# Performance work log

Measured on AMD Instinct MI355X. Metric: run time of the kernel, lower is better.

Reference implementation:

```python
import jax, jax.numpy as jnp
import numpy as np

B = 8192
N_CLASSES = 1024
MARGIN = 0.1
THRESH = 0.5
SCALE_POS = 2.0
SCALE_NEG = 40.0
EPS = 1e-5


def setup_inputs() -> dict:
    key = jax.random.key(0)
    k1, k2 = jax.random.split(key)
    # cosine-similarity-like values in [-1, 1]
    sim_mat = jax.random.uniform(k1, (B, B), dtype=jnp.float32, minval=-1.0, maxval=1.0)
    labels = jax.random.randint(k2, (B,), 0, N_CLASSES, dtype=jnp.int64)
    return {"sim_mat": sim_mat, "labels": labels}


def reference(sim_mat, labels):
    # [B, B] pair masks
    same = labels[:, None] == labels[None, :]
    pos_mask = same & (sim_mat < 1.0 - EPS)        # positives, excluding self-sim ~ 1
    neg_mask = ~same

    # per-row hardest positive (min) / hardest negative (max); inf sentinels when empty
    min_pos = jnp.min(jnp.where(pos_mask, sim_mat, jnp.inf), axis=1)   # [B]
    max_neg = jnp.max(jnp.where(neg_mask, sim_mat, -jnp.inf), axis=1)  # [B]

    # pair mining: keep informative pairs only
    sel_neg = neg_mask & (sim_mat + MARGIN > min_pos[:, None])
    sel_pos = pos_mask & (sim_mat - MARGIN < max_neg[:, None])

    valid = jnp.any(sel_neg, axis=1) & jnp.any(sel_pos, axis=1)  # rows contributing to loss

    # masked soft-plus style logsumexp losses (sim bounded in [-1,1], exp is safe)
    pos_sum = jnp.sum(jnp.where(sel_pos, jnp.exp(-SCALE_POS * (sim_mat - THRESH)), 0.0), axis=1)
    neg_sum = jnp.sum(jnp.where(sel_neg, jnp.exp(SCALE_NEG * (sim_mat - THRESH)), 0.0), axis=1)
    pos_loss = jnp.log1p(pos_sum) / SCALE_POS
    neg_loss = jnp.log1p(neg_sum) / SCALE_NEG

    loss = jnp.sum(jnp.where(valid, pos_loss + neg_loss, 0.0)) / sim_mat.shape[0]
    return loss
```

## Files before the change

kernel.cpp:

```cpp
#include <hip/hip_runtime.h>
#include <math.h>

namespace {
constexpr int   kB       = 8192;
constexpr int   kBlock   = 256;
constexpr int   kWaves   = kBlock / 64;
constexpr int   kRPW     = 2;
constexpr int   kGrid    = kB / (kWaves * kRPW);
constexpr int   kChunks  = kB / (64 * 4);
constexpr int   kNWaves  = kGrid * kWaves;
constexpr float kMargin   = 0.1f;
constexpr float kThresh   = 0.5f;
constexpr float kScalePos = 2.0f;
constexpr float kScaleNeg = 40.0f;
constexpr float kEps      = 1e-5f;
}

__global__ __launch_bounds__(kBlock, 2) void ms_rows_kernel(
    const float* __restrict__ sim,
    const int*   __restrict__ labels,
    float*       __restrict__ ws)
{
  const int tid  = threadIdx.x;
  const int wave = tid >> 6;
  const int lane = tid & 63;
  const int wid  = blockIdx.x * kWaves + wave;

  float wave_loss = 0.0f;

  #pragma unroll
  for (int rr = 0; rr < kRPW; ++rr) {
    const int row = wid * kRPW + rr;
    const int ml  = labels[row];
    const float* __restrict__ srow = sim + (size_t)row * kB;

    float4 buf[kChunks];
    #pragma unroll
    for (int k = 0; k < kChunks; ++k)
      buf[k] = *reinterpret_cast<const float4*>(srow + k * 256 + lane * 4);

    unsigned int msk[kChunks / 8] = {0, 0, 0, 0};
    float min_pos =  INFINITY;
    float max_neg = -INFINITY;
    #pragma unroll
    for (int k = 0; k < kChunks; ++k) {
      const int4   l4 = *reinterpret_cast<const int4*>(labels + k * 256 + lane * 4);
      const float4 v  = buf[k];
      const float xs[4] = {v.x, v.y, v.z, v.w};
      const int   ls[4] = {l4.x, l4.y, l4.z, l4.w};
      #pragma unroll
      for (int c = 0; c < 4; ++c) {
        const bool  same = (ls[c] == ml);
        msk[k >> 3] |= (unsigned)same << ((k & 7) * 4 + c);
        const float x = xs[c];
        min_pos = fminf(min_pos, (same && x < 1.0f - kEps) ? x : INFINITY);
        max_neg = fmaxf(max_neg, same ? -INFINITY : x);
      }
    }
    #pragma unroll
    for (int off = 32; off > 0; off >>= 1) {
      min_pos = fminf(min_pos, __shfl_xor(min_pos, off, 64));
      max_neg = fmaxf(max_neg, __shfl_xor(max_neg, off, 64));
    }

    float ps = 0.0f, ns = 0.0f;
    #pragma unroll
    for (int k = 0; k < kChunks; ++k) {
      const float4 v = buf[k];
      const float xs[4] = {v.x, v.y, v.z, v.w};
      #pragma unroll
      for (int c = 0; c < 4; ++c) {
        const bool  same = (msk[k >> 3] >> ((k & 7) * 4 + c)) & 1u;
        const float x = xs[c];
        const float a = same ? -kScalePos : kScaleNeg;
        const float e = __expf(a * (x - kThresh));
        ps += (same && x < 1.0f - kEps && x - kMargin < max_neg) ? e : 0.0f;
        ns += (!same && x + kMargin > min_pos) ? e : 0.0f;
      }
    }
    #pragma unroll
    for (int off = 32; off > 0; off >>= 1) {
      ps += __shfl_xor(ps, off, 64);
      ns += __shfl_xor(ns, off, 64);
    }
    if (ps > 0.0f && ns > 0.0f) {
      wave_loss += log1pf(ps) * (1.0f / kScalePos)
                 + log1pf(ns) * (1.0f / kScaleNeg);
    }
  }

  if (lane == 0) ws[wid] = wave_loss;
}

__global__ __launch_bounds__(256) void ms_reduce_kernel(
    const float* __restrict__ ws, float* __restrict__ out)
{
  const int tid = threadIdx.x;
  float s = 0.0f;
  #pragma unroll
  for (int i = tid; i < kNWaves; i += 256) s += ws[i];
  #pragma unroll
  for (int off = 32; off > 0; off >>= 1) s += __shfl_xor(s, off, 64);
  __shared__ float sm[4];
  if ((tid & 63) == 0) sm[tid >> 6] = s;
  __syncthreads();
  if (tid == 0)
    out[0] = (sm[0] + sm[1] + sm[2] + sm[3]) * (1.0f / (float)kB);
}

extern "C" void kernel_launch(void* const* d_in, const int* in_sizes, int n_in,
                              void* d_out, int out_size, void* d_ws, size_t ws_size,
                              hipStream_t stream) {
  const float* sim    = (const float*)d_in[0];
  const int*   labels = (const int*)d_in[1];
  float*       ws     = (float*)d_ws;
  float*       out    = (float*)d_out;

  ms_rows_kernel<<<dim3(kGrid), dim3(kBlock), 0, stream>>>(sim, labels, ws);
  ms_reduce_kernel<<<dim3(1), dim3(256), 0, stream>>>(ws, out);
}
```

Measured before the change: 432.9 us.

## Stream rows in double-buffered chunks and re-read them instead of holding whole rows

Each wave previously held an entire 8192-element row in registers (32 float4 per lane) across two passes. Now it handles one row, streams it in double-buffered chunks of 8 float4 for the min/max pass, then reloads the row from memory (likely L2/MALL hits) for the exp-sum pass. This cuts VGPR pressure so occupancy can rise (launch bounds raised to 4 blocks). The cost is reading the 256MB matrix twice, which doubles traffic if the reread misses cache.

```diff
diff --git a/kernel.cpp b/kernel.cpp
--- a/kernel.cpp
+++ b/kernel.cpp
@@ -5,10 +5,10 @@
 constexpr int   kB       = 8192;
 constexpr int   kBlock   = 256;
 constexpr int   kWaves   = kBlock / 64;
-constexpr int   kRPW     = 2;
-constexpr int   kGrid    = kB / (kWaves * kRPW);
-constexpr int   kChunks  = kB / (64 * 4);
-constexpr int   kNWaves  = kGrid * kWaves;
+constexpr int   kGrid    = kB / kWaves;
+constexpr int   kCF4     = 8;
+constexpr int   kChunkE  = 64 * 4 * kCF4;
+constexpr int   kNChunk  = kB / kChunkE;
 constexpr float kMargin   = 0.1f;
 constexpr float kThresh   = 0.5f;
 constexpr float kScalePos = 2.0f;
@@ -16,80 +16,108 @@
 constexpr float kEps      = 1e-5f;
 }
 
-__global__ __launch_bounds__(kBlock, 2) void ms_rows_kernel(
+__global__ __launch_bounds__(kBlock, 4) void ms_rows_kernel(
     const float* __restrict__ sim,
     const int*   __restrict__ labels,
     float*       __restrict__ ws)
 {
   const int tid  = threadIdx.x;
-  const int wave = tid >> 6;
   const int lane = tid & 63;
-  const int wid  = blockIdx.x * kWaves + wave;
+  const int row  = blockIdx.x * kWaves + (tid >> 6);
 
-  float wave_loss = 0.0f;
+  const int ml = labels[row];
+  const float* __restrict__ srow = sim + (size_t)row * kB;
+  const int base = lane * 4;
+
+  float4 buf[2][kCF4];
 
   #pragma unroll
-  for (int rr = 0; rr < kRPW; ++rr) {
-    const int row = wid * kRPW + rr;
-    const int ml  = labels[row];
-    const float* __restrict__ srow = sim + (size_t)row * kB;
+  for (int k = 0; k < kCF4; ++k)
+    buf[0][k] = *reinterpret_cast<const float4*>(srow + k * 256 + base);
 
-    float4 buf[kChunks];
+  unsigned int msk[kNChunk];
+  float min_pos =  INFINITY;
+  float max_neg = -INFINITY;
+
+  #pragma unroll
+  for (int c = 0; c < kNChunk; ++c) {
+    if (c + 1 < kNChunk) {
+      #pragma unroll
+      for (int k = 0; k < kCF4; ++k)
+        buf[(c + 1) & 1][k] = *reinterpret_cast<const float4*>(
+            srow + (c + 1) * kChunkE + k * 256 + base);
+    }
+    unsigned int m = 0;
     #pragma unroll
-    for (int k = 0; k < kChunks; ++k)
-      buf[k] = *reinterpret_cast<const float4*>(srow + k * 256 + lane * 4);
-
-    unsigned int msk[kChunks / 8] = {0, 0, 0, 0};
-    float min_pos =  INFINITY;
-    float max_neg = -INFINITY;
-    #pragma unroll
-    for (int k = 0; k < kChunks; ++k) {
-      const int4   l4 = *reinterpret_cast<const int4*>(labels + k * 256 + lane * 4);
-      const float4 v  = buf[k];
+    for (int k = 0; k < kCF4; ++k) {
+      const int4   l4 = *reinterpret_cast<const int4*>(labels + c * kChunkE + k * 256 + base);
+      const float4 v  = buf[c & 1][k];
       const float xs[4] = {v.x, v.y, v.z, v.w};
       const int   ls[4] = {l4.x, l4.y, l4.z, l4.w};
       #pragma unroll
-      for (int c = 0; c < 4; ++c) {
-        const bool  same = (ls[c] == ml);
-        msk[k >> 3] |= (unsigned)same << ((k & 7) * 4 + c);
-        const float x = xs[c];
+      for (int cc = 0; cc < 4; ++cc) {
+        const bool  same = (ls[cc] == ml);
+        m |= (unsigned)same << (k * 4 + cc);
+        const float x = xs[cc];
         min_pos = fminf(min_pos, (same && x < 1.0f - kEps) ? x : INFINITY);
         max_neg = fmaxf(max_neg, same ? -INFINITY : x);
       }
     }
+    msk[c] = m;
+  }
+
+  #pragma unroll
+  for (int off = 32; off > 0; off >>= 1) {
+    min_pos = fminf(min_pos, __shfl_xor(min_pos, off, 64));
+    max_neg = fmaxf(max_neg, __shfl_xor(max_neg, off, 64));
+  }
+
+  __builtin_amdgcn_sched_barrier(0);
+
+  #pragma unroll
+  for (int k = 0; k < kCF4; ++k)
+    buf[0][k] = *reinterpret_cast<const float4*>(srow + k * 256 + base);
+
+  float ps = 0.0f, ns = 0.0f;
+  #pragma unroll
+  for (int c = 0; c < kNChunk; ++c) {
+    if (c + 1 < kNChunk) {
+      #pragma unroll
+      for (int k = 0; k < kCF4; ++k)
+        buf[(c + 1) & 1][k] = *reinterpret_cast<const float4*>(
+            srow + (c + 1) * kChunkE + k * 256 + base);
+    }
+    const unsigned int m = msk[c];
     #pragma unroll
-    for (int off = 32; off > 0; off >>= 1) {
-      min_pos = fminf(min_pos, __shfl_xor(min_pos, off, 64));
-      max_neg = fmaxf(max_neg, __shfl_xor(max_neg, off, 64));
-    }
-
-    float ps = 0.0f, ns = 0.0f;
-    #pragma unroll
-    for (int k = 0; k < kChunks; ++k) {
-      const float4 v = buf[k];
+    for (int k = 0; k < kCF4; ++k) {
+      const float4 v = buf[c & 1][k];
       const float xs[4] = {v.x, v.y, v.z, v.w};
       #pragma unroll
-      for (int c = 0; c < 4; ++c) {
-        const bool  same = (msk[k >> 3] >> ((k & 7) * 4 + c)) & 1u;
-        const float x = xs[c];
+      for (int cc = 0; cc < 4; ++cc) {
+        const bool  same = (m >> (k * 4 + cc)) & 1u;
+        const float x = xs[cc];
         const float a = same ? -kScalePos : kScaleNeg;
         const float e = __expf(a * (x - kThresh));
         ps += (same && x < 1.0f - kEps && x - kMargin < max_neg) ? e : 0.0f;
         ns += (!same && x + kMargin > min_pos) ? e : 0.0f;
       }
     }
-    #pragma unroll
-    for (int off = 32; off > 0; off >>= 1) {
-      ps += __shfl_xor(ps, off, 64);
-      ns += __shfl_xor(ns, off, 64);
-    }
-    if (ps > 0.0f && ns > 0.0f) {
-      wave_loss += log1pf(ps) * (1.0f / kScalePos)
-                 + log1pf(ns) * (1.0f / kScaleNeg);
-    }
   }
 
-  if (lane == 0) ws[wid] = wave_loss;
+  #pragma unroll
+  for (int off = 32; off > 0; off >>= 1) {
+    ps += __shfl_xor(ps, off, 64);
+    ns += __shfl_xor(ns, off, 64);
+  }
+
+  if (lane == 0) {
+    float loss = 0.0f;
+    if (ps > 0.0f && ns > 0.0f) {
+      loss = log1pf(ps) * (1.0f / kScalePos)
+           + log1pf(ns) * (1.0f / kScaleNeg);
+    }
+    ws[row] = loss;
+  }
 }
 
 __global__ __launch_bounds__(256) void ms_reduce_kernel(
@@ -98,7 +126,7 @@
   const int tid = threadIdx.x;
   float s = 0.0f;
   #pragma unroll
-  for (int i = tid; i < kNWaves; i += 256) s += ws[i];
+  for (int i = tid; i < kB; i += 256) s += ws[i];
   #pragma unroll
   for (int off = 32; off > 0; off >>= 1) s += __shfl_xor(s, off, 64);
   __shared__ float sm[4];
```

Result: slower. 514.9 us (+18.9%).
